# Optimization experiments

Measured on AMD Instinct MI355X. Metric: run time of the kernel, lower is better.

Reference implementation:

```python
import math
import jax, jax.numpy as jnp
import numpy as np

FILTER_ORDER = 64
FILTER_EMB_DIM = 5
HIDDEN = 256
SHIFT = 0.05
FAST_DECAY_PCT = 0.3
SLOW_DECAY_PCT = 1.5
TARGET = 0.01


def setup_inputs() -> dict:
    key = jax.random.key(0)
    ks = jax.random.split(key, 8)
    B, C, L = 8, HIDDEN, 8192

    def lin_w(k, fan_out, fan_in):
        return jax.random.normal(k, (fan_out, fan_in), jnp.float32) / np.sqrt(fan_in).astype(np.float32)

    return {
        "x": jax.random.normal(ks[0], (B, C, L), jnp.float32),
        "W1": lin_w(ks[1], FILTER_ORDER, FILTER_EMB_DIM),
        "b1": jnp.zeros((FILTER_ORDER,), jnp.float32),
        "freq0": jnp.ones((1, FILTER_ORDER), jnp.float32),
        "W2": lin_w(ks[2], FILTER_ORDER, FILTER_ORDER),
        "b2": jnp.zeros((FILTER_ORDER,), jnp.float32),
        "freq1": jnp.ones((1, FILTER_ORDER), jnp.float32),
        "W3": lin_w(ks[3], FILTER_ORDER, FILTER_ORDER),
        "b3": jnp.zeros((FILTER_ORDER,), jnp.float32),
        "freq2": jnp.ones((1, FILTER_ORDER), jnp.float32),
        "Wout": lin_w(ks[4], HIDDEN, FILTER_ORDER),
        "D": jax.random.normal(ks[5], (HIDDEN,), jnp.float32),
        "L": L,
    }


def _pos_emb(L):
    # HyenaDnaPositionalEmbedding: z (1, L, emb_dim), t (1, L, 1)
    t = jnp.linspace(0.0, 1.0, L, dtype=jnp.float32)[None, :, None]
    t_rescaled = jnp.linspace(0.0, L - 1, L, dtype=jnp.float32)[None, :, None]
    w = 2.0 * math.pi * t_rescaled / L  # (1, L, 1)
    bands = (FILTER_EMB_DIM - 1) // 2
    f = jnp.linspace(1e-4, bands - 1, bands, dtype=jnp.float32)[None, None]  # (1, 1, bands)
    z = jnp.concatenate([t, jnp.cos(-f * w), jnp.sin(-f * w)], axis=-1)  # (1, L, emb_dim)
    return z, t


def _filter_kernel(W1, b1, freq0, W2, b2, freq1, W3, b3, freq2, Wout, L):
    z, t = _pos_emb(L)
    h = jnp.sin(freq0 * (jnp.einsum('ble,oe->blo', z, W1) + b1))
    h = jnp.sin(freq1 * (jnp.einsum('blo,po->blp', h, W2) + b2))
    h = jnp.sin(freq2 * (jnp.einsum('blo,po->blp', h, W3) + b3))
    h = jnp.einsum('blo,do->bld', h, Wout)  # (1, L, HIDDEN)
    # exponential modulation window
    max_decay = math.log(TARGET) / FAST_DECAY_PCT
    min_decay = math.log(TARGET) / SLOW_DECAY_PCT
    deltas = jnp.linspace(min_decay, max_decay, HIDDEN, dtype=jnp.float32)[None, None]
    decay = jnp.exp(-t * jnp.abs(deltas))  # (1, L, HIDDEN)
    h = h * (decay + SHIFT)
    return h[0].T  # (HIDDEN, L) channels-major kernel


def _fftconv(u, k, D):
    # y = conv(u, k) + u * D via FFT, zero-padded to 2L (linear convolution)
    L = u.shape[-1]
    fft_size = 2 * L
    k_f = jnp.fft.rfft(k.astype(jnp.float32), n=fft_size) / fft_size  # (C, fft_size//2+1)
    u_f = jnp.fft.rfft(u.astype(jnp.float32), n=fft_size)             # (B, C, fft_size//2+1)
    y = jnp.fft.irfft(u_f * k_f, n=fft_size, norm='forward')[..., :L]
    return (y + u * D[:, None]).astype(u.dtype)


def reference(x, W1, b1, freq0, W2, b2, freq1, W3, b3, freq2, Wout, D, L):
    k = _filter_kernel(W1, b1, freq0, W2, b2, freq1, W3, b3, freq2, Wout, L)
    return _fftconv(x, k, D)
```

## Files before the change

### kernel.cpp

```cpp
#include <hip/hip_runtime.h>

#define L_SEQ 8192
#define NTH 1024
#define HID 256
#define PIDX(i) ((i) + ((i) >> 4))
#define LDS_SZ 8704

#define ANG16 3.83495196971410315e-4f
#define CS16 0.99999992646571789f
#define SN16 3.83495187571395563e-4f
#define C707 0.70710678118654752f

__device__ float2 TWID[4088];
template<int M> struct TWOFF;
template<> struct TWOFF<512> { static constexpr int v = 0;    };
template<> struct TWOFF<64>  { static constexpr int v = 3584; };
template<> struct TWOFF<8>   { static constexpr int v = 4032; };

__global__ __launch_bounds__(256) void twid_kernel() {
  int g = blockIdx.x * 256 + threadIdx.x;
  float denom;
  int h;
  if (g < 3584)      { h = g;        denom = 4096.0f; }
  else if (g < 4032) { h = g - 3584; denom = 512.0f;  }
  else if (g < 4088) { h = g - 4032; denom = 64.0f;   }
  else return;
  int i = h / 7, j = h - 7*i + 1;
  float s, c;
  sincosf(-6.2831853071795864769f * (float)(i*j) / denom, &s, &c);
  TWID[g] = make_float2(c, s);
}

__device__ __forceinline__ float2 cmul(float2 a, float2 b) {
  return make_float2(a.x*b.x - a.y*b.y, a.x*b.y + a.y*b.x);
}
__device__ __forceinline__ float2 cadd(float2 a, float2 b){ return make_float2(a.x+b.x, a.y+b.y); }
__device__ __forceinline__ float2 csub(float2 a, float2 b){ return make_float2(a.x-b.x, a.y-b.y); }

__device__ __forceinline__ void bf4_fwd(float2 a0, float2 a1, float2 a2, float2 a3,
                                        float2& o0, float2& o1, float2& o2, float2& o3) {
  float2 t0 = cadd(a0,a2), t1 = csub(a0,a2), t2 = cadd(a1,a3), t3 = csub(a1,a3);
  o0 = cadd(t0,t2);
  o2 = csub(t0,t2);
  o1 = make_float2(t1.x + t3.y, t1.y - t3.x);
  o3 = make_float2(t1.x - t3.y, t1.y + t3.x);
}
__device__ __forceinline__ void bf4_inv(float2 c0, float2 c1, float2 c2, float2 c3,
                                        float2& o0, float2& o1, float2& o2, float2& o3) {
  float2 u0 = cadd(c0,c2), u2 = csub(c0,c2), u1 = cadd(c1,c3);
  float2 v3 = make_float2(c3.y - c1.y, c1.x - c3.x);
  o0 = cadd(u0,u1); o2 = csub(u0,u1); o1 = cadd(u2,v3); o3 = csub(u2,v3);
}

__device__ __forceinline__ void fwd8(float2 P[8]) {
  float2 e0=cadd(P[0],P[4]), e1=cadd(P[1],P[5]), e2=cadd(P[2],P[6]), e3=cadd(P[3],P[7]);
  float2 o0=csub(P[0],P[4]), o1=csub(P[1],P[5]), o2=csub(P[2],P[6]), o3=csub(P[3],P[7]);
  o1 = make_float2((o1.x+o1.y)*C707, (o1.y-o1.x)*C707);
  o2 = make_float2(o2.y, -o2.x);
  o3 = make_float2((o3.y-o3.x)*C707, -(o3.x+o3.y)*C707);
  float2 q0,q1,q2,q3;
  bf4_fwd(e0,e1,e2,e3,q0,q1,q2,q3);
  P[0]=q0; P[2]=q1; P[4]=q2; P[6]=q3;
  bf4_fwd(o0,o1,o2,o3,q0,q1,q2,q3);
  P[1]=q0; P[3]=q1; P[5]=q2; P[7]=q3;
}
__device__ __forceinline__ void inv8(float2 P[8]) {
  float2 E0,E1,E2,E3,O0,O1,O2,O3;
  bf4_inv(P[0],P[2],P[4],P[6],E0,E1,E2,E3);
  bf4_inv(P[1],P[3],P[5],P[7],O0,O1,O2,O3);
  O1 = make_float2((O1.x-O1.y)*C707, (O1.x+O1.y)*C707);
  O2 = make_float2(-O2.y, O2.x);
  O3 = make_float2(-(O3.x+O3.y)*C707, (O3.x-O3.y)*C707);
  P[0]=cadd(E0,O0); P[4]=csub(E0,O0);
  P[1]=cadd(E1,O1); P[5]=csub(E1,O1);
  P[2]=cadd(E2,O2); P[6]=csub(E2,O2);
  P[3]=cadd(E3,O3); P[7]=csub(E3,O3);
}

template<int M>
__device__ __forceinline__ void fwd_stage8_2(float2* __restrict__ X0,
                                             float2* __restrict__ X1, int t) {
  int i2 = t & (M-1);
  int g  = t / M;
  int base = g*8*M + i2;
  const float2* __restrict__ wp = TWID + TWOFF<M>::v + i2*7;
  float2 w[7];
  #pragma unroll
  for (int j=0;j<7;++j) w[j] = wp[j];
  {
    float2 P[8];
    #pragma unroll
    for (int j=0;j<8;++j) P[j] = X0[PIDX(base + j*M)];
    fwd8(P);
    X0[PIDX(base)] = P[0];
    #pragma unroll
    for (int j=1;j<8;++j) X0[PIDX(base + j*M)] = cmul(P[j], w[j-1]);
  }
  {
    float2 P[8];
    #pragma unroll
    for (int j=0;j<8;++j) P[j] = X1[PIDX(base + j*M)];
    fwd8(P);
    X1[PIDX(base)] = P[0];
    #pragma unroll
    for (int j=1;j<8;++j) X1[PIDX(base + j*M)] = cmul(P[j], w[j-1]);
  }
}
template<int M>
__device__ __forceinline__ void inv_stage8_2(float2* __restrict__ X0,
                                             float2* __restrict__ X1, int t) {
  int i2 = t & (M-1);
  int g  = t / M;
  int base = g*8*M + i2;
  const float2* __restrict__ wp = TWID + TWOFF<M>::v + i2*7;
  float2 w[7];
  #pragma unroll
  for (int j=0;j<7;++j) { float2 v = wp[j]; w[j] = make_float2(v.x, -v.y); }
  {
    float2 P[8];
    P[0] = X0[PIDX(base)];
    #pragma unroll
    for (int j=1;j<8;++j) P[j] = cmul(X0[PIDX(base + j*M)], w[j-1]);
    inv8(P);
    #pragma unroll
    for (int j=0;j<8;++j) X0[PIDX(base + j*M)] = P[j];
  }
  {
    float2 P[8];
    P[0] = X1[PIDX(base)];
    #pragma unroll
    for (int j=1;j<8;++j) P[j] = cmul(X1[PIDX(base + j*M)], w[j-1]);
    inv8(P);
    #pragma unroll
    for (int j=0;j<8;++j) X1[PIDX(base + j*M)] = P[j];
  }
}

__device__ __forceinline__ void fft_mid_fwd2(float2* __restrict__ X0,
                                             float2* __restrict__ X1, int t) {
  __syncthreads();
  fwd_stage8_2<512>(X0,X1,t); __syncthreads();
  fwd_stage8_2<64>(X0,X1,t);  __syncthreads();
  fwd_stage8_2<8>(X0,X1,t);   __syncthreads();
}
__device__ __forceinline__ void fft_mid_inv2(float2* __restrict__ X0,
                                             float2* __restrict__ X1, int t) {
  __syncthreads();
  inv_stage8_2<8>(X0,X1,t);   __syncthreads();
  inv_stage8_2<64>(X0,X1,t);  __syncthreads();
  inv_stage8_2<512>(X0,X1,t); __syncthreads();
}

__device__ __forceinline__ void middle_pointwise2(float2* __restrict__ X0,
                                                  float2* __restrict__ X1,
                                                  const float2* __restrict__ KA,
                                                  const float2* __restrict__ KB, int t) {
  int base = 8*t;
  {
    float2 k[8];
    #pragma unroll
    for (int q=0;q<8;++q) k[q] = KA[base+q];
    float2 P[8];
    #pragma unroll
    for (int q=0;q<8;++q) P[q] = X0[PIDX(base+q)];
    fwd8(P);
    #pragma unroll
    for (int q=0;q<8;++q) P[q] = cmul(P[q], k[q]);
    inv8(P);
    #pragma unroll
    for (int q=0;q<8;++q) X0[PIDX(base+q)] = P[q];
  }
  {
    float2 k[8];
    #pragma unroll
    for (int q=0;q<8;++q) k[q] = KB[base+q];
    float2 P[8];
    #pragma unroll
    for (int q=0;q<8;++q) P[q] = X1[PIDX(base+q)];
    fwd8(P);
    #pragma unroll
    for (int q=0;q<8;++q) P[q] = cmul(P[q], k[q]);
    inv8(P);
    #pragma unroll
    for (int q=0;q<8;++q) X1[PIDX(base+q)] = P[q];
  }
}

__global__ __launch_bounds__(256) void mlp_kernel(
    const float* __restrict__ W1, const float* __restrict__ b1, const float* __restrict__ fq0,
    const float* __restrict__ W2, const float* __restrict__ b2, const float* __restrict__ fq1,
    const float* __restrict__ W3, const float* __restrict__ b3, const float* __restrict__ fq2,
    float* __restrict__ h3g) {
  __shared__ float hs[2][16][64];
  int tid = threadIdx.x;
  int lane = tid & 63, w = tid >> 6;
  int l0 = blockIdx.x * 16;

  float w1r[5];
  #pragma unroll
  for (int e = 0; e < 5; ++e) w1r[e] = W1[lane*5+e];
  float b1v = b1[lane], f0 = fq0[lane];
  #pragma unroll
  for (int r = 0; r < 4; ++r) {
    int l = l0 + w + 4*r;
    float t = (float)l * (1.0f / (float)(L_SEQ - 1));
    float ang = 6.2831853071795864769f * (float)l / (float)L_SEQ;
    float s0, c0, s1, c1;
    __sincosf(1e-4f * ang, &s0, &c0);
    __sincosf(ang, &s1, &c1);
    float acc = b1v + t*w1r[0] + c0*w1r[1] + c1*w1r[2] - s0*w1r[3] - s1*w1r[4];
    hs[0][w + 4*r][lane] = __sinf(f0 * acc);
  }
  __syncthreads();

  float wr[64];
  #pragma unroll
  for (int j = 0; j < 16; ++j) *(float4*)&wr[4*j] = *(const float4*)&W2[lane*64 + 4*j];
  float b2v = b2[lane], f1 = fq1[lane];
  #pragma unroll
  for (int r = 0; r < 4; ++r) {
    int ll = w + 4*r;
    float a0 = 0.f, a1 = 0.f, a2 = 0.f, a3 = 0.f;
    #pragma unroll
    for (int o = 0; o < 64; o += 4) {
      a0 += hs[0][ll][o+0] * wr[o+0];
      a1 += hs[0][ll][o+1] * wr[o+1];
      a2 += hs[0][ll][o+2] * wr[o+2];
      a3 += hs[0][ll][o+3] * wr[o+3];
    }
    hs[1][ll][lane] = __sinf(f1 * (b2v + ((a0+a1)+(a2+a3))));
  }
  __syncthreads();

  #pragma unroll
  for (int j = 0; j < 16; ++j) *(float4*)&wr[4*j] = *(const float4*)&W3[lane*64 + 4*j];
  float b3v = b3[lane], f2 = fq2[lane];
  #pragma unroll
  for (int r = 0; r < 4; ++r) {
    int ll = w + 4*r;
    float a0 = 0.f, a1 = 0.f, a2 = 0.f, a3 = 0.f;
    #pragma unroll
    for (int o = 0; o < 64; o += 4) {
      a0 += hs[1][ll][o+0] * wr[o+0];
      a1 += hs[1][ll][o+1] * wr[o+1];
      a2 += hs[1][ll][o+2] * wr[o+2];
      a3 += hs[1][ll][o+3] * wr[o+3];
    }
    h3g[(size_t)(l0 + ll) * 64 + lane] = __sinf(f2 * (b3v + ((a0+a1)+(a2+a3))));
  }
}

__global__ __launch_bounds__(256) void kwrite_kernel(const float* __restrict__ h3g,
                                                     const float* __restrict__ Wout,
                                                     const float* __restrict__ Dv,
                                                     float* __restrict__ kbuf) {
  __shared__ float tileh[256][65];
  int tid = threadIdx.x;
  int l0 = blockIdx.x * 256;
  int c0 = blockIdx.y * 32;
  {
    const float4* src = (const float4*)(h3g + (size_t)l0 * 64);
    #pragma unroll
    for (int q = 0; q < 16; ++q) {
      int idx = tid + 256*q;
      int row = idx >> 4, col4 = idx & 15;
      float4 v = src[idx];
      tileh[row][col4*4+0] = v.x;
      tileh[row][col4*4+1] = v.y;
      tileh[row][col4*4+2] = v.z;
      tileh[row][col4*4+3] = v.w;
    }
  }
  __syncthreads();
  float hr[64];
  #pragma unroll
  for (int o = 0; o < 64; ++o) hr[o] = tileh[tid][o];
  int l = l0 + tid;
  float t = (float)l * (1.0f / (float)(L_SEQ - 1));
  const float mind = -3.0701134573253945f;
  const float maxd = -15.350567286626972f;
  for (int jj = 0; jj < 32; ++jj) {
    int c = c0 + jj;
    float a0 = 0.f, a1 = 0.f, a2 = 0.f, a3 = 0.f;
    #pragma unroll
    for (int o = 0; o < 64; o += 4) {
      a0 += hr[o+0] * Wout[c*64+o+0];
      a1 += hr[o+1] * Wout[c*64+o+1];
      a2 += hr[o+2] * Wout[c*64+o+2];
      a3 += hr[o+3] * Wout[c*64+o+3];
    }
    float acc = (a0+a1)+(a2+a3);
    float delta = mind + (maxd - mind) * ((float)c * (1.0f/255.0f));
    float dec = __expf(-t * fabsf(delta)) + 0.05f;
    float v = acc * dec;
    if (l == 0) v += Dv[c];
    kbuf[(size_t)c * L_SEQ + l] = v;
  }
}

__global__ __launch_bounds__(NTH) void kf_kernel(const float* __restrict__ kbuf,
                                                 float2* __restrict__ Kf) {
  __shared__ float2 X0[LDS_SZ];
  __shared__ float2 X1[LDS_SZ];
  int c = blockIdx.x;
  int t = threadIdx.x;
  const float* kr = kbuf + (size_t)c * L_SEQ;
  const float sc = 1.0f / 16384.0f;
  {
    int n0 = 4*t;
    float4 lo4 = *(const float4*)(kr + n0);
    float4 hi4 = *(const float4*)(kr + n0 + 4096);
    float s16, c16; __sincosf(-ANG16 * (float)n0, &s16, &c16);
    float2 w16 = make_float2(c16, s16);
    #pragma unroll
    for (int j = 0; j < 4; ++j) {
      if (j) w16 = cmul(w16, make_float2(CS16, -SN16));
      float2 w8 = cmul(w16, w16);
      float klo = ((const float*)&lo4)[j];
      float khi = ((const float*)&hi4)[j];
      X0[PIDX(n0+j)]      = make_float2(klo + khi, 0.f);
      float d = klo - khi;
      X0[PIDX(n0+j+4096)] = make_float2(d * w8.x, d * w8.y);
      float2 vlo = make_float2(klo * w16.x, klo * w16.y);
      float2 vhi = make_float2(khi * w16.y, -khi * w16.x);
      X1[PIDX(n0+j)]      = cadd(vlo, vhi);
      X1[PIDX(n0+j+4096)] = cmul(csub(vlo, vhi), w8);
    }
  }
  fft_mid_fwd2(X0, X1, t);
  {
    int base = 8*t;
    float2* out0 = Kf + (size_t)c * 16384 + base;
    float2* out1 = out0 + 8192;
    {
      float2 P[8];
      #pragma unroll
      for (int q=0;q<8;++q) P[q] = X0[PIDX(base+q)];
      fwd8(P);
      #pragma unroll
      for (int q=0;q<8;++q) out0[q] = make_float2(P[q].x*sc, P[q].y*sc);
    }
    {
      float2 P[8];
      #pragma unroll
      for (int q=0;q<8;++q) P[q] = X1[PIDX(base+q)];
      fwd8(P);
      #pragma unroll
      for (int q=0;q<8;++q) out1[q] = make_float2(P[q].x*sc, P[q].y*sc);
    }
  }
}

__global__ __launch_bounds__(NTH) void conv_kernel(const float* __restrict__ x,
                                                   const float2* __restrict__ Kf,
                                                   float* __restrict__ y) {
  __shared__ float2 X0[LDS_SZ];
  __shared__ float2 X1[LDS_SZ];
  int c = blockIdx.x;
  int p = blockIdx.y;
  int t = threadIdx.x;
  const float* u0 = x + ((size_t)p       * HID + c) * L_SEQ;
  const float* u1 = x + ((size_t)(p + 4) * HID + c) * L_SEQ;
  const float2* KA = Kf + (size_t)c * 16384;
  const float2* KB = KA + 8192;
  float* y0 = y + ((size_t)p       * HID + c) * L_SEQ;
  float* y1 = y + ((size_t)(p + 4) * HID + c) * L_SEQ;

  {
    int n0 = 4*t;
    float4 a0 = *(const float4*)(u0 + n0);
    float4 a1 = *(const float4*)(u1 + n0);
    float4 b0 = *(const float4*)(u0 + n0 + 4096);
    float4 b1 = *(const float4*)(u1 + n0 + 4096);
    float sb, cb; __sincosf(-ANG16 * (float)n0, &sb, &cb);
    float2 w16 = make_float2(cb, sb);
    #pragma unroll
    for (int j = 0; j < 4; ++j) {
      if (j) w16 = cmul(w16, make_float2(CS16, -SN16));
      float2 w8 = cmul(w16, w16);
      float2 vlo = make_float2(((const float*)&a0)[j], ((const float*)&a1)[j]);
      float2 vhi = make_float2(((const float*)&b0)[j], ((const float*)&b1)[j]);
      X0[PIDX(n0+j)]      = cadd(vlo, vhi);
      X0[PIDX(n0+j+4096)] = cmul(csub(vlo, vhi), w8);
      float2 vloB = cmul(vlo, w16);
      float2 vhiB = cmul(vhi, make_float2(w16.y, -w16.x));
      X1[PIDX(n0+j)]      = cadd(vloB, vhiB);
      X1[PIDX(n0+j+4096)] = cmul(csub(vloB, vhiB), w8);
    }
  }
  fft_mid_fwd2(X0, X1, t);
  middle_pointwise2(X0, X1, KA, KB, t);
  fft_mid_inv2(X0, X1, t);
  {
    int n0 = 4*t;
    float sb, cb; __sincosf(ANG16 * (float)n0, &sb, &cb);
    float2 w16b = make_float2(cb, sb);
    float4 w00, w01, w10, w11;
    #pragma unroll
    for (int j = 0; j < 4; ++j) {
      if (j) w16b = cmul(w16b, make_float2(CS16, SN16));
      float2 w8b = cmul(w16b, w16b);
      float2 P0 = X0[PIDX(n0+j)], Q0 = X0[PIDX(n0+j+4096)];
      float2 P1 = X1[PIDX(n0+j)], Q1 = X1[PIDX(n0+j+4096)];
      float2 tt0 = cmul(Q0, w8b);
      float2 tt1 = cmul(Q1, w8b);
      float2 lo = cadd(cadd(P0, tt0), cmul(cadd(P1, tt1), w16b));
      float2 hi = cadd(csub(P0, tt0), cmul(csub(P1, tt1), make_float2(-w16b.y, w16b.x)));
      ((float*)&w00)[j] = lo.x; ((float*)&w01)[j] = lo.y;
      ((float*)&w10)[j] = hi.x; ((float*)&w11)[j] = hi.y;
    }
    *(float4*)(y0 + n0)        = w00;
    *(float4*)(y1 + n0)        = w01;
    *(float4*)(y0 + n0 + 4096) = w10;
    *(float4*)(y1 + n0 + 4096) = w11;
  }
}

extern "C" void kernel_launch(void* const* d_in, const int* in_sizes, int n_in,
                              void* d_out, int out_size, void* d_ws, size_t ws_size,
                              hipStream_t stream) {
  const float* x    = (const float*)d_in[0];
  const float* W1   = (const float*)d_in[1];
  const float* b1   = (const float*)d_in[2];
  const float* fq0  = (const float*)d_in[3];
  const float* W2   = (const float*)d_in[4];
  const float* b2   = (const float*)d_in[5];
  const float* fq1  = (const float*)d_in[6];
  const float* W3   = (const float*)d_in[7];
  const float* b3   = (const float*)d_in[8];
  const float* fq2  = (const float*)d_in[9];
  const float* Wout = (const float*)d_in[10];
  const float* Dv   = (const float*)d_in[11];

  float*  kbuf = (float*)d_ws;
  float2* Kf   = (float2*)((char*)d_ws + (size_t)HID * L_SEQ * sizeof(float));
  float*  h3g  = (float*)((char*)d_ws + 38ull*1024*1024);
  float*  y    = (float*)d_out;

  twid_kernel  <<<dim3(16),    256, 0, stream>>>();
  mlp_kernel   <<<dim3(512),   256, 0, stream>>>(W1,b1,fq0,W2,b2,fq1,W3,b3,fq2,h3g);
  kwrite_kernel<<<dim3(32, 8), 256, 0, stream>>>(h3g, Wout, Dv, kbuf);
  kf_kernel    <<<dim3(256),    NTH, 0, stream>>>(kbuf, Kf);
  conv_kernel  <<<dim3(256, 4), NTH, 0, stream>>>(x, Kf, y);
}
```

Before: 140.9 us.

## Split convolution into two half-spectrum kernels to halve LDS per block

The single conv kernel, which held two 8192-point LDS buffers per block (even and odd frequency halves), becomes a templated kernel handling one half at a time. It is launched twice: the odd half writes y, then the even half reads y back and accumulates. This halves LDS per block, allowing more resident blocks per CU. The cost is reading x twice and writing/reading y an extra time through global memory, plus a second launch.

```diff
diff --git a/kernel.cpp b/kernel.cpp
--- a/kernel.cpp
+++ b/kernel.cpp
@@ -7,8 +7,11 @@
 #define LDS_SZ 8704
 
 #define ANG16 3.83495196971410315e-4f
+#define ANG8  7.66990393942820630e-4f
 #define CS16 0.99999992646571789f
 #define SN16 3.83495187571395563e-4f
+#define CS8  0.99999970586287223f
+#define SN8  7.66990318742704490e-4f
 #define C707 0.70710678118654752f
 
 __device__ float2 TWID[4088];
@@ -78,8 +81,7 @@
 }
 
 template<int M>
-__device__ __forceinline__ void fwd_stage8_2(float2* __restrict__ X0,
-                                             float2* __restrict__ X1, int t) {
+__device__ __forceinline__ void fwd_stage8(float2* __restrict__ X, int t) {
   int i2 = t & (M-1);
   int g  = t / M;
   int base = g*8*M + i2;
@@ -87,28 +89,16 @@
   float2 w[7];
   #pragma unroll
   for (int j=0;j<7;++j) w[j] = wp[j];
-  {
-    float2 P[8];
-    #pragma unroll
-    for (int j=0;j<8;++j) P[j] = X0[PIDX(base + j*M)];
-    fwd8(P);
-    X0[PIDX(base)] = P[0];
-    #pragma unroll
-    for (int j=1;j<8;++j) X0[PIDX(base + j*M)] = cmul(P[j], w[j-1]);
-  }
-  {
-    float2 P[8];
-    #pragma unroll
-    for (int j=0;j<8;++j) P[j] = X1[PIDX(base + j*M)];
-    fwd8(P);
-    X1[PIDX(base)] = P[0];
-    #pragma unroll
-    for (int j=1;j<8;++j) X1[PIDX(base + j*M)] = cmul(P[j], w[j-1]);
-  }
+  float2 P[8];
+  #pragma unroll
+  for (int j=0;j<8;++j) P[j] = X[PIDX(base + j*M)];
+  fwd8(P);
+  X[PIDX(base)] = P[0];
+  #pragma unroll
+  for (int j=1;j<8;++j) X[PIDX(base + j*M)] = cmul(P[j], w[j-1]);
 }
 template<int M>
-__device__ __forceinline__ void inv_stage8_2(float2* __restrict__ X0,
-                                             float2* __restrict__ X1, int t) {
+__device__ __forceinline__ void inv_stage8(float2* __restrict__ X, int t) {
   int i2 = t & (M-1);
   int g  = t / M;
   int base = g*8*M + i2;
@@ -116,74 +106,43 @@
   float2 w[7];
   #pragma unroll
   for (int j=0;j<7;++j) { float2 v = wp[j]; w[j] = make_float2(v.x, -v.y); }
-  {
-    float2 P[8];
-    P[0] = X0[PIDX(base)];
-    #pragma unroll
-    for (int j=1;j<8;++j) P[j] = cmul(X0[PIDX(base + j*M)], w[j-1]);
-    inv8(P);
-    #pragma unroll
-    for (int j=0;j<8;++j) X0[PIDX(base + j*M)] = P[j];
-  }
-  {
-    float2 P[8];
-    P[0] = X1[PIDX(base)];
-    #pragma unroll
-    for (int j=1;j<8;++j) P[j] = cmul(X1[PIDX(base + j*M)], w[j-1]);
-    inv8(P);
-    #pragma unroll
-    for (int j=0;j<8;++j) X1[PIDX(base + j*M)] = P[j];
-  }
-}
-
-__device__ __forceinline__ void fft_mid_fwd2(float2* __restrict__ X0,
-                                             float2* __restrict__ X1, int t) {
-  __syncthreads();
-  fwd_stage8_2<512>(X0,X1,t); __syncthreads();
-  fwd_stage8_2<64>(X0,X1,t);  __syncthreads();
-  fwd_stage8_2<8>(X0,X1,t);   __syncthreads();
-}
-__device__ __forceinline__ void fft_mid_inv2(float2* __restrict__ X0,
-                                             float2* __restrict__ X1, int t) {
-  __syncthreads();
-  inv_stage8_2<8>(X0,X1,t);   __syncthreads();
-  inv_stage8_2<64>(X0,X1,t);  __syncthreads();
-  inv_stage8_2<512>(X0,X1,t); __syncthreads();
-}
-
-__device__ __forceinline__ void middle_pointwise2(float2* __restrict__ X0,
-                                                  float2* __restrict__ X1,
-                                                  const float2* __restrict__ KA,
-                                                  const float2* __restrict__ KB, int t) {
+  float2 P[8];
+  P[0] = X[PIDX(base)];
+  #pragma unroll
+  for (int j=1;j<8;++j) P[j] = cmul(X[PIDX(base + j*M)], w[j-1]);
+  inv8(P);
+  #pragma unroll
+  for (int j=0;j<8;++j) X[PIDX(base + j*M)] = P[j];
+}
+
+__device__ __forceinline__ void fft_mid_fwd(float2* __restrict__ X, int t) {
+  __syncthreads();
+  fwd_stage8<512>(X,t); __syncthreads();
+  fwd_stage8<64>(X,t);  __syncthreads();
+  fwd_stage8<8>(X,t);   __syncthreads();
+}
+__device__ __forceinline__ void fft_mid_inv(float2* __restrict__ X, int t) {
+  __syncthreads();
+  inv_stage8<8>(X,t);   __syncthreads();
+  inv_stage8<64>(X,t);  __syncthreads();
+  inv_stage8<512>(X,t); __syncthreads();
+}
+
+__device__ __forceinline__ void middle_pointwise(float2* __restrict__ X,
+                                                 const float2* __restrict__ K, int t) {
   int base = 8*t;
-  {
-    float2 k[8];
-    #pragma unroll
-    for (int q=0;q<8;++q) k[q] = KA[base+q];
-    float2 P[8];
-    #pragma unroll
-    for (int q=0;q<8;++q) P[q] = X0[PIDX(base+q)];
-    fwd8(P);
-    #pragma unroll
-    for (int q=0;q<8;++q) P[q] = cmul(P[q], k[q]);
-    inv8(P);
-    #pragma unroll
-    for (int q=0;q<8;++q) X0[PIDX(base+q)] = P[q];
-  }
-  {
-    float2 k[8];
-    #pragma unroll
-    for (int q=0;q<8;++q) k[q] = KB[base+q];
-    float2 P[8];
-    #pragma unroll
-    for (int q=0;q<8;++q) P[q] = X1[PIDX(base+q)];
-    fwd8(P);
-    #pragma unroll
-    for (int q=0;q<8;++q) P[q] = cmul(P[q], k[q]);
-    inv8(P);
-    #pragma unroll
-    for (int q=0;q<8;++q) X1[PIDX(base+q)] = P[q];
-  }
+  float2 k[8];
+  #pragma unroll
+  for (int q=0;q<8;++q) k[q] = K[base+q];
+  float2 P[8];
+  #pragma unroll
+  for (int q=0;q<8;++q) P[q] = X[PIDX(base+q)];
+  fwd8(P);
+  #pragma unroll
+  for (int q=0;q<8;++q) P[q] = cmul(P[q], k[q]);
+  inv8(P);
+  #pragma unroll
+  for (int q=0;q<8;++q) X[PIDX(base+q)] = P[q];
 }
 
 __global__ __launch_bounds__(256) void mlp_kernel(
@@ -327,7 +286,10 @@
       X1[PIDX(n0+j+4096)] = cmul(csub(vlo, vhi), w8);
     }
   }
-  fft_mid_fwd2(X0, X1, t);
+  __syncthreads();
+  fwd_stage8<512>(X0,t); fwd_stage8<512>(X1,t); __syncthreads();
+  fwd_stage8<64>(X0,t);  fwd_stage8<64>(X1,t);  __syncthreads();
+  fwd_stage8<8>(X0,t);   fwd_stage8<8>(X1,t);   __syncthreads();
   {
     int base = 8*t;
     float2* out0 = Kf + (size_t)c * 16384 + base;
@@ -351,18 +313,17 @@
   }
 }
 
-__global__ __launch_bounds__(NTH) void conv_kernel(const float* __restrict__ x,
-                                                   const float2* __restrict__ Kf,
-                                                   float* __restrict__ y) {
-  __shared__ float2 X0[LDS_SZ];
-  __shared__ float2 X1[LDS_SZ];
+template<int PIPE>
+__global__ __launch_bounds__(NTH) void conv_pipe(const float* __restrict__ x,
+                                                 const float2* __restrict__ Kf,
+                                                 float* __restrict__ y) {
+  __shared__ float2 X[LDS_SZ];
   int c = blockIdx.x;
   int p = blockIdx.y;
   int t = threadIdx.x;
   const float* u0 = x + ((size_t)p       * HID + c) * L_SEQ;
   const float* u1 = x + ((size_t)(p + 4) * HID + c) * L_SEQ;
-  const float2* KA = Kf + (size_t)c * 16384;
-  const float2* KB = KA + 8192;
+  const float2* K = Kf + (size_t)c * 16384 + PIPE*8192;
   float* y0 = y + ((size_t)p       * HID + c) * L_SEQ;
   float* y1 = y + ((size_t)(p + 4) * HID + c) * L_SEQ;
 
@@ -372,47 +333,80 @@
     float4 a1 = *(const float4*)(u1 + n0);
     float4 b0 = *(const float4*)(u0 + n0 + 4096);
     float4 b1 = *(const float4*)(u1 + n0 + 4096);
-    float sb, cb; __sincosf(-ANG16 * (float)n0, &sb, &cb);
-    float2 w16 = make_float2(cb, sb);
-    #pragma unroll
-    for (int j = 0; j < 4; ++j) {
-      if (j) w16 = cmul(w16, make_float2(CS16, -SN16));
-      float2 w8 = cmul(w16, w16);
-      float2 vlo = make_float2(((const float*)&a0)[j], ((const float*)&a1)[j]);
-      float2 vhi = make_float2(((const float*)&b0)[j], ((const float*)&b1)[j]);
-      X0[PIDX(n0+j)]      = cadd(vlo, vhi);
-      X0[PIDX(n0+j+4096)] = cmul(csub(vlo, vhi), w8);
-      float2 vloB = cmul(vlo, w16);
-      float2 vhiB = cmul(vhi, make_float2(w16.y, -w16.x));
-      X1[PIDX(n0+j)]      = cadd(vloB, vhiB);
-      X1[PIDX(n0+j+4096)] = cmul(csub(vloB, vhiB), w8);
-    }
-  }
-  fft_mid_fwd2(X0, X1, t);
-  middle_pointwise2(X0, X1, KA, KB, t);
-  fft_mid_inv2(X0, X1, t);
+    if (PIPE == 0) {
+      float sb, cb; __sincosf(-ANG8 * (float)n0, &sb, &cb);
+      float2 w8 = make_float2(cb, sb);
+      #pragma unroll
+      for (int j = 0; j < 4; ++j) {
+        if (j) w8 = cmul(w8, make_float2(CS8, -SN8));
+        float2 vlo = make_float2(((const float*)&a0)[j], ((const float*)&a1)[j]);
+        float2 vhi = make_float2(((const float*)&b0)[j], ((const float*)&b1)[j]);
+        X[PIDX(n0+j)]      = cadd(vlo, vhi);
+        X[PIDX(n0+j+4096)] = cmul(csub(vlo, vhi), w8);
+      }
+    } else {
+      float sb, cb; __sincosf(-ANG16 * (float)n0, &sb, &cb);
+      float2 w16 = make_float2(cb, sb);
+      #pragma unroll
+      for (int j = 0; j < 4; ++j) {
+        if (j) w16 = cmul(w16, make_float2(CS16, -SN16));
+        float2 w8 = cmul(w16, w16);
+        float2 vlo = cmul(make_float2(((const float*)&a0)[j], ((const float*)&a1)[j]), w16);
+        float2 vhi = cmul(make_float2(((const float*)&b0)[j], ((const float*)&b1)[j]),
+                          make_float2(w16.y, -w16.x));
+        X[PIDX(n0+j)]      = cadd(vlo, vhi);
+        X[PIDX(n0+j+4096)] = cmul(csub(vlo, vhi), w8);
+      }
+    }
+  }
+  fft_mid_fwd(X, t);
+  middle_pointwise(X, K, t);
+  fft_mid_inv(X, t);
   {
     int n0 = 4*t;
-    float sb, cb; __sincosf(ANG16 * (float)n0, &sb, &cb);
-    float2 w16b = make_float2(cb, sb);
     float4 w00, w01, w10, w11;
-    #pragma unroll
-    for (int j = 0; j < 4; ++j) {
-      if (j) w16b = cmul(w16b, make_float2(CS16, SN16));
-      float2 w8b = cmul(w16b, w16b);
-      float2 P0 = X0[PIDX(n0+j)], Q0 = X0[PIDX(n0+j+4096)];
-      float2 P1 = X1[PIDX(n0+j)], Q1 = X1[PIDX(n0+j+4096)];
-      float2 tt0 = cmul(Q0, w8b);
-      float2 tt1 = cmul(Q1, w8b);
-      float2 lo = cadd(cadd(P0, tt0), cmul(cadd(P1, tt1), w16b));
-      float2 hi = cadd(csub(P0, tt0), cmul(csub(P1, tt1), make_float2(-w16b.y, w16b.x)));
-      ((float*)&w00)[j] = lo.x; ((float*)&w01)[j] = lo.y;
-      ((float*)&w10)[j] = hi.x; ((float*)&w11)[j] = hi.y;
-    }
-    *(float4*)(y0 + n0)        = w00;
-    *(float4*)(y1 + n0)        = w01;
-    *(float4*)(y0 + n0 + 4096) = w10;
-    *(float4*)(y1 + n0 + 4096) = w11;
+    if (PIPE == 1) {
+      float sb, cb; __sincosf(ANG16 * (float)n0, &sb, &cb);
+      float2 w16b = make_float2(cb, sb);
+      #pragma unroll
+      for (int j = 0; j < 4; ++j) {
+        if (j) w16b = cmul(w16b, make_float2(CS16, SN16));
+        float2 w8b = cmul(w16b, w16b);
+        float2 P = X[PIDX(n0+j)], Q = X[PIDX(n0+j+4096)];
+        float2 tt = cmul(Q, w8b);
+        float2 lo = cmul(cadd(P, tt), w16b);
+        float2 hi = cmul(csub(P, tt), make_float2(-w16b.y, w16b.x));
+        ((float*)&w00)[j] = lo.x; ((float*)&w01)[j] = lo.y;
+        ((float*)&w10)[j] = hi.x; ((float*)&w11)[j] = hi.y;
+      }
+      *(float4*)(y0 + n0)        = w00;
+      *(float4*)(y1 + n0)        = w01;
+      *(float4*)(y0 + n0 + 4096) = w10;
+      *(float4*)(y1 + n0 + 4096) = w11;
+    } else {
+      float4 p00 = *(const float4*)(y0 + n0);
+      float4 p01 = *(const float4*)(y1 + n0);
+      float4 p10 = *(const float4*)(y0 + n0 + 4096);
+      float4 p11 = *(const float4*)(y1 + n0 + 4096);
+      float sb, cb; __sincosf(ANG8 * (float)n0, &sb, &cb);
+      float2 w8b = make_float2(cb, sb);
+      #pragma unroll
+      for (int j = 0; j < 4; ++j) {
+        if (j) w8b = cmul(w8b, make_float2(CS8, SN8));
+        float2 P = X[PIDX(n0+j)], Q = X[PIDX(n0+j+4096)];
+        float2 tt = cmul(Q, w8b);
+        float2 lo = cadd(P, tt);
+        float2 hi = csub(P, tt);
+        ((float*)&w00)[j] = lo.x + ((const float*)&p00)[j];
+        ((float*)&w01)[j] = lo.y + ((const float*)&p01)[j];
+        ((float*)&w10)[j] = hi.x + ((const float*)&p10)[j];
+        ((float*)&w11)[j] = hi.y + ((const float*)&p11)[j];
+      }
+      *(float4*)(y0 + n0)        = w00;
+      *(float4*)(y1 + n0)        = w01;
+      *(float4*)(y0 + n0 + 4096) = w10;
+      *(float4*)(y1 + n0 + 4096) = w11;
+    }
   }
 }
 
@@ -441,5 +435,6 @@
   mlp_kernel   <<<dim3(512),   256, 0, stream>>>(W1,b1,fq0,W2,b2,fq1,W3,b3,fq2,h3g);
   kwrite_kernel<<<dim3(32, 8), 256, 0, stream>>>(h3g, Wout, Dv, kbuf);
   kf_kernel    <<<dim3(256),    NTH, 0, stream>>>(kbuf, Kf);
-  conv_kernel  <<<dim3(256, 4), NTH, 0, stream>>>(x, Kf, y);
-}
+  conv_pipe<1> <<<dim3(256, 4), NTH, 0, stream>>>(x, Kf, y);
+  conv_pipe<0> <<<dim3(256, 4), NTH, 0, stream>>>(x, Kf, y);
+}
```

Result: slower. 173.0 us (+22.8%).

## Split filter FFT kernel into two blocks per channel, one per half-spectrum pipe

Applied to the files above, without the earlier changes.

The filter-spectrum kernel previously ran both half-spectrum FFT pipelines in one block with two LDS buffers. Each block now handles a single pipe selected by blockIdx.x, using one LDS buffer, which doubles the block count and halves per-block LDS. The global PIDX padding also changes from every 16 to every 8 elements, which affects LDS bank-conflict behaviour in all kernels, including conv_kernel. In exchange, each kbuf row is read twice, and the larger padding raises LDS usage in conv_kernel, which may cut its occupancy.

```diff
diff --git a/kernel.cpp b/kernel.cpp
--- a/kernel.cpp
+++ b/kernel.cpp
@@ -3,12 +3,15 @@
 #define L_SEQ 8192
 #define NTH 1024
 #define HID 256
-#define PIDX(i) ((i) + ((i) >> 4))
-#define LDS_SZ 8704
+#define PIDX(i) ((i) + ((i) >> 3))
+#define LDS_SZ 9216
 
 #define ANG16 3.83495196971410315e-4f
+#define ANG8  7.66990393942820630e-4f
 #define CS16 0.99999992646571789f
 #define SN16 3.83495187571395563e-4f
+#define CS8  0.99999970586287223f
+#define SN8  7.66990318742704490e-4f
 #define C707 0.70710678118654752f
 
 __device__ float2 TWID[4088];
@@ -78,6 +81,24 @@
 }
 
 template<int M>
+__device__ __forceinline__ void fwd_stage8(float2* __restrict__ X, int t) {
+  int i2 = t & (M-1);
+  int g  = t / M;
+  int base = g*8*M + i2;
+  const float2* __restrict__ wp = TWID + TWOFF<M>::v + i2*7;
+  float2 w[7];
+  #pragma unroll
+  for (int j=0;j<7;++j) w[j] = wp[j];
+  float2 P[8];
+  #pragma unroll
+  for (int j=0;j<8;++j) P[j] = X[PIDX(base + j*M)];
+  fwd8(P);
+  X[PIDX(base)] = P[0];
+  #pragma unroll
+  for (int j=1;j<8;++j) X[PIDX(base + j*M)] = cmul(P[j], w[j-1]);
+}
+
+template<int M>
 __device__ __forceinline__ void fwd_stage8_2(float2* __restrict__ X0,
                                              float2* __restrict__ X1, int t) {
   int i2 = t & (M-1);
@@ -300,9 +321,9 @@
 
 __global__ __launch_bounds__(NTH) void kf_kernel(const float* __restrict__ kbuf,
                                                  float2* __restrict__ Kf) {
-  __shared__ float2 X0[LDS_SZ];
-  __shared__ float2 X1[LDS_SZ];
-  int c = blockIdx.x;
+  __shared__ float2 X[LDS_SZ];
+  int pipe = blockIdx.x;
+  int c = blockIdx.y;
   int t = threadIdx.x;
   const float* kr = kbuf + (size_t)c * L_SEQ;
   const float sc = 1.0f / 16384.0f;
@@ -310,44 +331,47 @@
     int n0 = 4*t;
     float4 lo4 = *(const float4*)(kr + n0);
     float4 hi4 = *(const float4*)(kr + n0 + 4096);
-    float s16, c16; __sincosf(-ANG16 * (float)n0, &s16, &c16);
-    float2 w16 = make_float2(c16, s16);
-    #pragma unroll
-    for (int j = 0; j < 4; ++j) {
-      if (j) w16 = cmul(w16, make_float2(CS16, -SN16));
-      float2 w8 = cmul(w16, w16);
-      float klo = ((const float*)&lo4)[j];
-      float khi = ((const float*)&hi4)[j];
-      X0[PIDX(n0+j)]      = make_float2(klo + khi, 0.f);
-      float d = klo - khi;
-      X0[PIDX(n0+j+4096)] = make_float2(d * w8.x, d * w8.y);
-      float2 vlo = make_float2(klo * w16.x, klo * w16.y);
-      float2 vhi = make_float2(khi * w16.y, -khi * w16.x);
-      X1[PIDX(n0+j)]      = cadd(vlo, vhi);
-      X1[PIDX(n0+j+4096)] = cmul(csub(vlo, vhi), w8);
-    }
-  }
-  fft_mid_fwd2(X0, X1, t);
+    if (pipe == 0) {
+      float sb, cb; __sincosf(-ANG8 * (float)n0, &sb, &cb);
+      float2 w8 = make_float2(cb, sb);
+      #pragma unroll
+      for (int j = 0; j < 4; ++j) {
+        if (j) w8 = cmul(w8, make_float2(CS8, -SN8));
+        float klo = ((const float*)&lo4)[j];
+        float khi = ((const float*)&hi4)[j];
+        X[PIDX(n0+j)]      = make_float2(klo + khi, 0.f);
+        float d = klo - khi;
+        X[PIDX(n0+j+4096)] = make_float2(d * w8.x, d * w8.y);
+      }
+    } else {
+      float sb, cb; __sincosf(-ANG16 * (float)n0, &sb, &cb);
+      float2 w16 = make_float2(cb, sb);
+      #pragma unroll
+      for (int j = 0; j < 4; ++j) {
+        if (j) w16 = cmul(w16, make_float2(CS16, -SN16));
+        float klo = ((const float*)&lo4)[j];
+        float khi = ((const float*)&hi4)[j];
+        float2 vlo = make_float2(klo * w16.x, klo * w16.y);
+        float2 vhi = make_float2(khi * w16.y, -khi * w16.x);
+        float2 w8 = cmul(w16, w16);
+        X[PIDX(n0+j)]      = cadd(vlo, vhi);
+        X[PIDX(n0+j+4096)] = cmul(csub(vlo, vhi), w8);
+      }
+    }
+  }
+  __syncthreads();
+  fwd_stage8<512>(X,t); __syncthreads();
+  fwd_stage8<64>(X,t);  __syncthreads();
+  fwd_stage8<8>(X,t);   __syncthreads();
   {
     int base = 8*t;
-    float2* out0 = Kf + (size_t)c * 16384 + base;
-    float2* out1 = out0 + 8192;
-    {
-      float2 P[8];
-      #pragma unroll
-      for (int q=0;q<8;++q) P[q] = X0[PIDX(base+q)];
-      fwd8(P);
-      #pragma unroll
-      for (int q=0;q<8;++q) out0[q] = make_float2(P[q].x*sc, P[q].y*sc);
-    }
-    {
-      float2 P[8];
-      #pragma unroll
-      for (int q=0;q<8;++q) P[q] = X1[PIDX(base+q)];
-      fwd8(P);
-      #pragma unroll
-      for (int q=0;q<8;++q) out1[q] = make_float2(P[q].x*sc, P[q].y*sc);
-    }
+    float2 P[8];
+    #pragma unroll
+    for (int q=0;q<8;++q) P[q] = X[PIDX(base+q)];
+    fwd8(P);
+    float2* out = Kf + (size_t)c * 16384 + pipe*8192 + base;
+    #pragma unroll
+    for (int q=0;q<8;++q) out[q] = make_float2(P[q].x*sc, P[q].y*sc);
   }
 }
 
@@ -440,6 +464,6 @@
   twid_kernel  <<<dim3(16),    256, 0, stream>>>();
   mlp_kernel   <<<dim3(512),   256, 0, stream>>>(W1,b1,fq0,W2,b2,fq1,W3,b3,fq2,h3g);
   kwrite_kernel<<<dim3(32, 8), 256, 0, stream>>>(h3g, Wout, Dv, kbuf);
-  kf_kernel    <<<dim3(256),    NTH, 0, stream>>>(kbuf, Kf);
+  kf_kernel    <<<dim3(2, 256), NTH, 0, stream>>>(kbuf, Kf);
   conv_kernel  <<<dim3(256, 4), NTH, 0, stream>>>(x, Kf, y);
 }
```

New measurement: 145.6 us. +3.3%, slower.
